# Kernel optimization log

Measured on AMD Instinct MI355X. Metric: run time of the kernel, lower is better.

## Reference

```python
import jax, jax.numpy as jnp
import numpy as np

B, T, S = 64, 48, 48
E, H, L, V = 512, 1024, 2, 32000


def setup_inputs() -> dict:
    key = jax.random.key(0)
    ks = jax.random.split(key, 16)
    s = 0.02
    return {
        "tgt_input": jax.random.randint(ks[0], (B, T), 0, V),
        "h0": jax.random.normal(ks[1], (L, B, H), jnp.float32),
        "c0": jax.random.normal(ks[2], (L, B, H), jnp.float32),
        "encoder_output": jax.random.normal(ks[3], (B, S, H), jnp.float32),
        "src_key_padding_mask": jnp.zeros((B, S), bool),
        "embedding": jax.random.normal(ks[4], (V, E), jnp.float32) * s,
        "W_l": jax.random.normal(ks[5], (H, H), jnp.float32) * s,
        "b_l": jnp.zeros((H,), jnp.float32),
        "W_ih0": jax.random.normal(ks[6], (4 * H, E + H), jnp.float32) * s,
        "W_hh0": jax.random.normal(ks[7], (4 * H, H), jnp.float32) * s,
        "b_ih0": jnp.zeros((4 * H,), jnp.float32),
        "b_hh0": jnp.zeros((4 * H,), jnp.float32),
        "W_ih1": jax.random.normal(ks[8], (4 * H, H), jnp.float32) * s,
        "W_hh1": jax.random.normal(ks[9], (4 * H, H), jnp.float32) * s,
        "b_ih1": jnp.zeros((4 * H,), jnp.float32),
        "b_hh1": jnp.zeros((4 * H,), jnp.float32),
    }


def _lstm_cell(x, h, c, W_ih, W_hh, b_ih, b_hh):
    # PyTorch gate order: i, f, g, o
    gates = x @ W_ih.T + b_ih + h @ W_hh.T + b_hh  # [B, 4H]
    i, f, g, o = jnp.split(gates, 4, axis=-1)
    c_new = jax.nn.sigmoid(f) * c + jax.nn.sigmoid(i) * jnp.tanh(g)
    h_new = jax.nn.sigmoid(o) * jnp.tanh(c_new)
    return h_new, c_new


def reference(tgt_input, h0, c0, encoder_output, src_key_padding_mask,
              embedding, W_l, b_l,
              W_ih0, W_hh0, b_ih0, b_hh0,
              W_ih1, W_hh1, b_ih1, b_hh1):
    emb = embedding[tgt_input]              # [B, T, E]
    emb_t = jnp.transpose(emb, (1, 0, 2))   # [T, B, E]
    layers = ((W_ih0, W_hh0, b_ih0, b_hh0), (W_ih1, W_hh1, b_ih1, b_hh1))

    def step(carry, x_t):
        h, c = carry                        # [L, B, H] each
        # Luong attention with query = last-layer hidden state
        q = h[-1] @ W_l.T + b_l             # [B, H]
        scores = jnp.einsum('bh,bsh->bs', q, encoder_output)
        scores = jnp.where(src_key_padding_mask, -jnp.inf, scores)
        attn = jax.nn.softmax(scores, axis=-1)
        ctx = jnp.einsum('bs,bsh->bh', attn, encoder_output)  # [B, H]
        x = jnp.concatenate([x_t, ctx], axis=-1)              # [B, E+H]
        new_h, new_c = [], []
        for l, (W_ih, W_hh, b_ih, b_hh) in enumerate(layers):
            hn, cn = _lstm_cell(x, h[l], c[l], W_ih, W_hh, b_ih, b_hh)
            new_h.append(hn)
            new_c.append(cn)
            x = hn
        return (jnp.stack(new_h), jnp.stack(new_c)), x  # x = top-layer output

    (hn, cn), outs = jax.lax.scan(step, (h0, c0), emb_t)
    outputs = jnp.transpose(outs, (1, 0, 2))  # [B, T, H]
    return outputs, hn, cn
```

## Files before the change

kernel.cpp:

```cpp
#include <hip/hip_runtime.h>
#include <stdint.h>


using short8 = __attribute__((ext_vector_type(8))) short;
using f32x4  = __attribute__((ext_vector_type(4))) float;
typedef unsigned short u16;
typedef unsigned long long u64;

#define B_  64
#define T_  48
#define S_  48
#define H_  1024
#define E_  512

__device__ __forceinline__ float bf2f(u16 u) {
    union { unsigned int i; float f; } v; v.i = ((unsigned int)u) << 16; return v.f;
}
__device__ __forceinline__ u16 f2bf(float f) {
    union { float f; unsigned int i; } v; v.f = f;
    unsigned int r = v.i + 0x7fff + ((v.i >> 16) & 1);
    return (u16)(r >> 16);
}
__device__ __forceinline__ float sigm(float x) { return 1.f / (1.f + __expf(-x)); }


__global__ void cast_copy(u16* __restrict__ dst, int dld, int doff,
                          const float* __restrict__ src, int sld, int soff,
                          int rows, int colshift) {
    int cols = 1 << colshift;
    int total = rows << colshift;
    for (int i = blockIdx.x * blockDim.x + threadIdx.x; i < total;
         i += gridDim.x * blockDim.x) {
        int r = i >> colshift, c = i & (cols - 1);
        dst[(size_t)r * dld + doff + c] = f2bf(src[(size_t)r * sld + soff + c]);
    }
}

__global__ void transpose_cast(u16* __restrict__ dst, const float* __restrict__ src) {
    int idx = blockIdx.x * blockDim.x + threadIdx.x;
    int r = idx >> 10, c = idx & 1023;
    dst[idx] = f2bf(src[(size_t)c * 1024 + r]);
}

__global__ void embed_gather(u16* __restrict__ embA, const float* __restrict__ emb,
                             const int* __restrict__ tgt) {
    int row = blockIdx.x;
    int t = row >> 6, b = row & 63;
    int id = tgt[b * T_ + t];
    const float* s = emb + (size_t)id * E_;
    u16* d = embA + (size_t)row * E_;
    for (int e = threadIdx.x; e < E_; e += blockDim.x) d[e] = f2bf(s[e]);
}

__global__ void sbias_kernel(float* __restrict__ sbias, const float* __restrict__ enc,
                             const float* __restrict__ b_l) {
    int r = blockIdx.x, lane = threadIdx.x;
    const float* e = enc + (size_t)r * H_;
    float acc = 0.f;
    for (int k = lane; k < H_; k += 64) acc += b_l[k] * e[k];
    for (int o = 32; o; o >>= 1) acc += __shfl_xor(acc, o);
    if (lane == 0) sbias[r] = acc;
}

__global__ void init_state(u16* __restrict__ xa0_0, u16* __restrict__ xa1_0,
                           const float* __restrict__ h0) {
    int i = blockIdx.x * blockDim.x + threadIdx.x;
    int l = i >> 16, rem = i & 65535, b = rem >> 10, c = rem & 1023;
    u16 hb = f2bf(h0[i]);
    if (l == 0) xa0_0[b * 2048 + 1024 + c] = hb;
    else        xa1_0[b * 2048 + 1024 + c] = hb;
}

__global__ __launch_bounds__(256) void gemm64(
    const u16* __restrict__ A, const u16* __restrict__ W, u16* __restrict__ D,
    const float* __restrict__ bias1, const float* __restrict__ bias2,
    int N, int Kd)
{
    __shared__ float part[4][64][65];
    int tid = threadIdx.x, w = tid >> 6, lane = tid & 63;
    int hf = lane >> 4, q = lane & 15;
    int n0 = blockIdx.x * 64, m0 = blockIdx.y * 64;
    int ks = Kd >> 2;
    int kb = w * ks + hf * 8;
    const u16* ap = A + (size_t)(m0 + q) * Kd + kb;
    const u16* wp = W + (size_t)(n0 + q) * Kd + kb;
    f32x4 acc[4][4] = {};
    for (int k0 = 0; k0 < ks; k0 += 32) {
        short8 bf[4], af[4];
#pragma unroll
        for (int n = 0; n < 4; ++n) bf[n] = *(const short8*)(wp + (size_t)n * 16 * Kd + k0);
#pragma unroll
        for (int m = 0; m < 4; ++m) af[m] = *(const short8*)(ap + (size_t)m * 16 * Kd + k0);
#pragma unroll
        for (int m = 0; m < 4; ++m)
#pragma unroll
            for (int n = 0; n < 4; ++n)
                acc[m][n] = __builtin_amdgcn_mfma_f32_16x16x32_bf16(af[m], bf[n], acc[m][n], 0, 0, 0);
    }
#pragma unroll
    for (int m = 0; m < 4; ++m)
#pragma unroll
        for (int n = 0; n < 4; ++n)
#pragma unroll
            for (int r = 0; r < 4; ++r)
                part[w][m * 16 + hf * 4 + r][n * 16 + q] = acc[m][n][r];
    __syncthreads();
#pragma unroll
    for (int k = 0; k < 16; ++k) {
        int o = tid + k * 256;
        int row = o >> 6, col = o & 63;
        float v = part[0][row][col] + part[1][row][col]
                + part[2][row][col] + part[3][row][col];
        if (bias1) v += bias1[n0 + col] + bias2[n0 + col];
        D[(size_t)(m0 + row) * N + n0 + col] = f2bf(v);
    }
}


struct PParams {
    const float *W_ih0, *W_hh0, *W_ih1, *W_hh1;
    const u16  *preG, *encW, *encB;
    const float *sbias, *b_ih1, *b_hh1, *c0in;
    const unsigned char* mask;
    u16 *XA0, *XA1;
    float *out, *hn0, *hn1, *cn0, *cn1;
    unsigned *cnt, *flags;
};

__device__ __forceinline__ void gridarrive(unsigned* cnt, int ep, int g) {
    __syncthreads();
    if (threadIdx.x == 0)
        __hip_atomic_fetch_add(&cnt[g * 256 + ep], 1u,
                               __ATOMIC_RELAXED, __HIP_MEMORY_SCOPE_AGENT);
    asm volatile("" ::: "memory");
}
__device__ __forceinline__ void gridpoll(unsigned* cnt, unsigned* flags,
                                         int ep, int g) {
    if (blockIdx.x == 0) {
        if (threadIdx.x < 64) {
            int spin = 0;
            for (;;) {
                unsigned v = __hip_atomic_load(&cnt[threadIdx.x * 256 + ep],
                                               __ATOMIC_RELAXED,
                                               __HIP_MEMORY_SCOPE_AGENT);
                if (__ballot(v >= 4u) == ~0ull) break;
                if (++spin > (1 << 20)) break;
            }
            __hip_atomic_store(&flags[threadIdx.x * 256 + ep], 1u,
                               __ATOMIC_RELAXED, __HIP_MEMORY_SCOPE_AGENT);
        }
    } else if (threadIdx.x == 0) {
        int spin = 0;
        while (!__hip_atomic_load(&flags[g * 256 + ep], __ATOMIC_RELAXED,
                                  __HIP_MEMORY_SCOPE_AGENT)) {
            if (++spin > (1 << 20)) break;
        }
    }
    asm volatile("" ::: "memory");
    __syncthreads();
}

__global__ void __launch_bounds__(256, 1) decoder_persistent(PParams P) {
    __shared__ u16 wlds[2][4096][8];
    __shared__ union {
        struct { float h1f[1056]; float sc[48][4]; float pr[48]; } at;
        float gates[64][20];
    } sm;

    const int tid = threadIdx.x, blk = blockIdx.x;
    const int w = tid >> 6, lane = tid & 63, g4 = lane >> 4, q = lane & 15;
    const int b2 = tid >> 2, j2 = tid & 3;
    const int colg = blk * 4 + j2;

    {
        int r = tid & 15, cb = tid >> 4;
        int grow = (r >> 2) * 1024 + blk * 4 + (r & 3);
#pragma unroll
        for (int l = 0; l < 2; ++l) {
            const float* Sa = l ? P.W_ih1 : P.W_ih0;
            const float* Sb = l ? P.W_hh1 : P.W_hh0;
            int sld  = l ? 1024 : 1536;
            int soff = l ? 0 : 512;
            for (int it = 0; it < 16; ++it) {
                int c = cb + it * 16;
                int k = c * 8;
                const float* src = (k < 1024)
                    ? (Sa + (size_t)grow * sld + soff + k)
                    : (Sb + (size_t)grow * 1024 + (k - 1024));
                float4 x0 = *(const float4*)(src);
                float4 x1 = *(const float4*)(src + 4);
                short8 v;
                v[0] = f2bf(x0.x); v[1] = f2bf(x0.y); v[2] = f2bf(x0.z); v[3] = f2bf(x0.w);
                v[4] = f2bf(x1.x); v[5] = f2bf(x1.y); v[6] = f2bf(x1.z); v[7] = f2bf(x1.w);
                *(short8*)&wlds[l][c * 16 + r][0] = v;
            }
        }
    }
    __syncthreads();
    float bsum[4];
#pragma unroll
    for (int g = 0; g < 4; ++g)
        bsum[g] = P.b_ih1[g * 1024 + colg] + P.b_hh1[g * 1024 + colg];
    float c0r = P.c0in[b2 * 1024 + colg];
    float c1r = P.c0in[65536 + b2 * 1024 + colg];

    const int ab = (blk & 7) * 8 + ((blk >> 3) & 7);
    const int aq = blk >> 6;
    int ep = 0;
    int t = 0;

    auto gemm_half = [&](const u16* Abase, int layer, int kbase, f32x4 seed) -> f32x4 {
        const u16* ap = Abase + (size_t)(w * 16 + q) * 2048 + kbase + g4 * 8;
        short8 xa[32];
#pragma unroll
        for (int kk = 0; kk < 32; ++kk)
            xa[kk] = *(const short8*)(ap + kk * 32);
        f32x4 a0 = seed, a1 = {}, a2 = {}, a3 = {};
        const int cbs = (kbase >> 3) + g4;
#pragma unroll
        for (int kk = 0; kk < 32; kk += 4) {
            a0 = __builtin_amdgcn_mfma_f32_16x16x32_bf16(
                xa[kk + 0], *(const short8*)&wlds[layer][(cbs + (kk + 0) * 4) * 16 + q][0], a0, 0, 0, 0);
            a1 = __builtin_amdgcn_mfma_f32_16x16x32_bf16(
                xa[kk + 1], *(const short8*)&wlds[layer][(cbs + (kk + 1) * 4) * 16 + q][0], a1, 0, 0, 0);
            a2 = __builtin_amdgcn_mfma_f32_16x16x32_bf16(
                xa[kk + 2], *(const short8*)&wlds[layer][(cbs + (kk + 2) * 4) * 16 + q][0], a2, 0, 0, 0);
            a3 = __builtin_amdgcn_mfma_f32_16x16x32_bf16(
                xa[kk + 3], *(const short8*)&wlds[layer][(cbs + (kk + 3) * 4) * 16 + q][0], a3, 0, 0, 0);
        }
        return (a0 + a1) + (a2 + a3);
    };

    auto lstm_phase = [&](const u16* Abase, int layer, f32x4 seed,
                          float add0, float add1, float add2, float add3,
                          float& creg, u16* dA, u16* dB, float* outp,
                          float* hnO, float* cnO, int doLast) {
        f32x4 g = gemm_half(Abase, layer, 0, seed);
#pragma unroll
        for (int r = 0; r < 4; ++r) sm.gates[w * 16 + g4 * 4 + r][q] = g[r];
        __syncthreads();
        float gi = sm.gates[b2][j2]      + add0;
        float gf = sm.gates[b2][4 + j2]  + add1;
        float gg = sm.gates[b2][8 + j2]  + add2;
        float go = sm.gates[b2][12 + j2] + add3;
        float cnew = sigm(gf) * creg + sigm(gi) * tanhf(gg);
        float hnew = sigm(go) * tanhf(cnew);
        creg = cnew;
        ((u16*)&sm.gates[b2][16])[j2] = f2bf(hnew);
        if (outp) outp[(size_t)(b2 * T_ + t) * H_ + colg] = hnew;
        if (doLast) { hnO[b2 * 1024 + colg] = hnew; cnO[b2 * 1024 + colg] = cnew; }
        __syncthreads();
        if (tid < 64) {
            u64 pk;
            __builtin_memcpy(&pk, (const u16*)&sm.gates[tid][16], 8);
            __hip_atomic_store((u64*)(dA + tid * 2048 + blk * 4), pk,
                               __ATOMIC_RELAXED, __HIP_MEMORY_SCOPE_AGENT);
            if (dB)
                __hip_atomic_store((u64*)(dB + tid * 2048 + blk * 4), pk,
                                   __ATOMIC_RELAXED, __HIP_MEMORY_SCOPE_AGENT);
        }
    };

    f32x4 g0p = gemm_half(P.XA0, 0, 1024, f32x4{});
    f32x4 g1p = {};

    for (t = 0; t < T_; ++t) {
        const int last = (t == T_ - 1);
        u16* xa0c = P.XA0 + (size_t)t * 131072;
        u16* xa0n = P.XA0 + (size_t)(t + 1) * 131072;
        u16* xa1c = P.XA1 + (size_t)t * 131072;
        u16* xa1n = P.XA1 + (size_t)(t + 1) * 131072;

        for (int i = tid; i < H_; i += 256)
            sm.at.h1f[(i >> 8) * 264 + (i & 255)] = bf2f(xa1c[ab * 2048 + 1024 + i]);
        __syncthreads();
        if (tid < 192) {
            int s = tid >> 2, kq = tid & 3;
            const u16* ew = P.encW + ((size_t)ab * S_ + s) * H_ + kq * 256;
            const float2* hp = (const float2*)(sm.at.h1f + kq * 264);
            float p0 = 0.f, p1 = 0.f, p2 = 0.f, p3 = 0.f;
#pragma unroll
            for (int k = 0; k < 256; k += 32) {
                short8 v0 = *(const short8*)(ew + k);
                short8 v1 = *(const short8*)(ew + k + 8);
                short8 v2 = *(const short8*)(ew + k + 16);
                short8 v3 = *(const short8*)(ew + k + 24);
#pragma unroll
                for (int e = 0; e < 8; e += 2) {
                    float2 h0v = hp[(k >> 1) + (e >> 1)];
                    p0 += h0v.x * bf2f(((u16*)&v0)[e]) + h0v.y * bf2f(((u16*)&v0)[e + 1]);
                    float2 h1v = hp[(k >> 1) + 4 + (e >> 1)];
                    p1 += h1v.x * bf2f(((u16*)&v1)[e]) + h1v.y * bf2f(((u16*)&v1)[e + 1]);
                    float2 h2v = hp[(k >> 1) + 8 + (e >> 1)];
                    p2 += h2v.x * bf2f(((u16*)&v2)[e]) + h2v.y * bf2f(((u16*)&v2)[e + 1]);
                    float2 h3v = hp[(k >> 1) + 12 + (e >> 1)];
                    p3 += h3v.x * bf2f(((u16*)&v3)[e]) + h3v.y * bf2f(((u16*)&v3)[e + 1]);
                }
            }
            sm.at.sc[s][kq] = (p0 + p1) + (p2 + p3);
        }
        __syncthreads();
        if (tid < 64) {
            float v = -3.0e38f;
            if (tid < S_) {
                v = sm.at.sc[tid][0] + sm.at.sc[tid][1] + sm.at.sc[tid][2]
                  + sm.at.sc[tid][3] + P.sbias[ab * S_ + tid];
                if (P.mask[ab * S_ + tid]) v = -3.0e38f;
            }
            float mx = v;
            for (int o = 32; o; o >>= 1) mx = fmaxf(mx, __shfl_xor(mx, o));
            float e = (tid < S_) ? __expf(v - mx) : 0.f;
            float su = e;
            for (int o = 32; o; o >>= 1) su += __shfl_xor(su, o);
            if (tid < S_) sm.at.pr[tid] = e / su;
        }
        __syncthreads();
        {
            int col = aq * 256 + tid;
            const u16* eb = P.encB + (size_t)ab * S_ * H_ + col;
            float a0 = 0.f, a1 = 0.f, a2 = 0.f, a3 = 0.f;
#pragma unroll
            for (int s = 0; s < 48; s += 4) {
                a0 += sm.at.pr[s + 0] * bf2f(eb[(size_t)(s + 0) * H_]);
                a1 += sm.at.pr[s + 1] * bf2f(eb[(size_t)(s + 1) * H_]);
                a2 += sm.at.pr[s + 2] * bf2f(eb[(size_t)(s + 2) * H_]);
                a3 += sm.at.pr[s + 3] * bf2f(eb[(size_t)(s + 3) * H_]);
            }
            u16 myb = f2bf((a0 + a1) + (a2 + a3));
            int other = __shfl_xor((int)myb, 1);
            if ((tid & 1) == 0) {
                unsigned pk = (unsigned)myb | ((unsigned)(u16)other << 16);
                __hip_atomic_store((unsigned*)(xa0c + ab * 2048 + col), pk,
                                   __ATOMIC_RELAXED, __HIP_MEMORY_SCOPE_AGENT);
            }
        }
        gridarrive(P.cnt, ++ep, ab);
        const u16* pgp = P.preG + ((size_t)t * 64 + b2) * 4096 + colg;
        u16 pg0 = pgp[0], pg1 = pgp[1024], pg2 = pgp[2048], pg3 = pgp[3072];
        gridpoll(P.cnt, P.flags, ep, ab);

        lstm_phase(xa0c, 0, g0p, bf2f(pg0), bf2f(pg1), bf2f(pg2), bf2f(pg3),
                   c0r, xa1c, xa0n + 1024, nullptr, P.hn0, P.cn0, last);
        gridarrive(P.cnt, ++ep, ab);
        g1p = gemm_half(xa1c, 1, 1024, f32x4{});
        gridpoll(P.cnt, P.flags, ep, ab);

        lstm_phase(xa1c, 1, g1p, bsum[0], bsum[1], bsum[2], bsum[3],
                   c1r, xa1n + 1024, nullptr, P.out, P.hn1, P.cn1, last);
        gridarrive(P.cnt, ++ep, ab);
        g0p = gemm_half(xa0n, 0, 1024, f32x4{});
        gridpoll(P.cnt, P.flags, ep, ab);
    }
}


extern "C" void kernel_launch(void* const* d_in, const int* in_sizes, int n_in,
                              void* d_out, int out_size, void* d_ws, size_t ws_size,
                              hipStream_t stream) {
    const int*   tgt      = (const int*)d_in[0];
    const float* h0       = (const float*)d_in[1];
    const float* c0in     = (const float*)d_in[2];
    const float* enc      = (const float*)d_in[3];
    const unsigned char* mask = (const unsigned char*)d_in[4];
    const float* embedding= (const float*)d_in[5];
    const float* W_l      = (const float*)d_in[6];
    const float* b_l      = (const float*)d_in[7];
    const float* W_ih0    = (const float*)d_in[8];
    const float* W_hh0    = (const float*)d_in[9];
    const float* b_ih0    = (const float*)d_in[10];
    const float* b_hh0    = (const float*)d_in[11];
    const float* W_ih1    = (const float*)d_in[12];
    const float* W_hh1    = (const float*)d_in[13];
    const float* b_ih1    = (const float*)d_in[14];
    const float* b_hh1    = (const float*)d_in[15];
    float* out = (float*)d_out;

    char* ws = (char*)d_ws;
    u16* W0emb = (u16*)ws;               ws += (size_t)4096 * 512 * 2;
    u16* WlT   = (u16*)ws;               ws += (size_t)1024 * 1024 * 2;
    u16* embA  = (u16*)ws;               ws += (size_t)3072 * 512 * 2;
    u16* encB  = (u16*)ws;               ws += (size_t)3072 * 1024 * 2;
    u16* encWb = (u16*)ws;               ws += (size_t)3072 * 1024 * 2;
    float* sbias = (float*)ws;           ws += (size_t)3072 * 4;
    u16* preG  = (u16*)ws;               ws += (size_t)3072 * 4096 * 2;
    u16* XA0   = (u16*)ws;               ws += (size_t)49 * 131072 * 2;
    u16* XA1   = (u16*)ws;               ws += (size_t)49 * 131072 * 2;
    unsigned* bar = (unsigned*)ws;       ws += 262144;

    cast_copy<<<2048, 256, 0, stream>>>(W0emb, 512, 0, W_ih0, 1536, 0, 4096, 9);
    cast_copy<<<2048, 256, 0, stream>>>(encB, 1024, 0, enc, 1024, 0, 3072, 10);
    transpose_cast<<<4096, 256, 0, stream>>>(WlT, W_l);
    embed_gather<<<3072, 256, 0, stream>>>(embA, embedding, tgt);
    init_state<<<512, 256, 0, stream>>>(XA0, XA1, h0);
    sbias_kernel<<<3072, 64, 0, stream>>>(sbias, enc, b_l);
    gemm64<<<dim3(64, 48), 256, 0, stream>>>(embA, W0emb, preG, b_ih0, b_hh0, 4096, 512);
    gemm64<<<dim3(16, 48), 256, 0, stream>>>(encB, WlT, encWb, nullptr, nullptr, 1024, 1024);
    hipMemsetAsync(bar, 0, 262144, stream);

    PParams prm;
    prm.W_ih0 = W_ih0; prm.W_hh0 = W_hh0; prm.W_ih1 = W_ih1; prm.W_hh1 = W_hh1;
    prm.preG = preG; prm.encW = encWb; prm.encB = encB;
    prm.sbias = sbias; prm.b_ih1 = b_ih1; prm.b_hh1 = b_hh1; prm.c0in = c0in;
    prm.mask = mask;
    prm.XA0 = XA0; prm.XA1 = XA1;
    prm.out = out;
    prm.hn0 = out + 3145728; prm.hn1 = out + 3145728 + 65536;
    prm.cn0 = out + 3276800; prm.cn1 = out + 3276800 + 65536;
    prm.cnt = bar; prm.flags = bar + 16384;
    decoder_persistent<<<256, 256, 0, stream>>>(prm);

    (void)in_sizes; (void)n_in; (void)out_size; (void)ws_size;
}
```

Baseline: 1.322 ms.

## Replace master-block barrier with hierarchical atomic counter and overlap layer-1 GEMM

The grid barrier drops the scheme where block 0 polls 64 group counters and writes per-group flags. Instead, the last arriving block of each 4-block group increments a global counter that every block polls directly, removing one relay hop per barrier. The layer-1 hidden-state GEMM (gemm_half on xa1c) is moved earlier so it runs while waiting at the attention barrier, and the barrier that used to follow it is left with nothing to hide. This adds contention on a single polled counter and relies on xa1c already being complete at that point.

Result: slower. 1.482 ms (+12.1%).

```diff
diff --git a/kernel.cpp b/kernel.cpp
--- a/kernel.cpp
+++ b/kernel.cpp
@@ -124,35 +124,27 @@
     const unsigned char* mask;
     u16 *XA0, *XA1;
     float *out, *hn0, *hn1, *cn0, *cn1;
-    unsigned *cnt, *flags;
+    unsigned *cnt, *gcnt;
 };
 
-__device__ __forceinline__ void gridarrive(unsigned* cnt, int ep, int g) {
+__device__ __forceinline__ void gridarrive(unsigned* cnt, unsigned* gcnt,
+                                           int ep, int g) {
     __syncthreads();
-    if (threadIdx.x == 0)
-        __hip_atomic_fetch_add(&cnt[g * 256 + ep], 1u,
-                               __ATOMIC_RELAXED, __HIP_MEMORY_SCOPE_AGENT);
+    if (threadIdx.x == 0) {
+        unsigned old = __hip_atomic_fetch_add(&cnt[g * 256 + ep], 1u,
+                                              __ATOMIC_RELAXED,
+                                              __HIP_MEMORY_SCOPE_AGENT);
+        if (old == 3u)
+            __hip_atomic_fetch_add(&gcnt[ep * 16], 1u,
+                                   __ATOMIC_RELAXED, __HIP_MEMORY_SCOPE_AGENT);
+    }
     asm volatile("" ::: "memory");
 }
-__device__ __forceinline__ void gridpoll(unsigned* cnt, unsigned* flags,
-                                         int ep, int g) {
-    if (blockIdx.x == 0) {
-        if (threadIdx.x < 64) {
-            int spin = 0;
-            for (;;) {
-                unsigned v = __hip_atomic_load(&cnt[threadIdx.x * 256 + ep],
-                                               __ATOMIC_RELAXED,
-                                               __HIP_MEMORY_SCOPE_AGENT);
-                if (__ballot(v >= 4u) == ~0ull) break;
-                if (++spin > (1 << 20)) break;
-            }
-            __hip_atomic_store(&flags[threadIdx.x * 256 + ep], 1u,
-                               __ATOMIC_RELAXED, __HIP_MEMORY_SCOPE_AGENT);
-        }
-    } else if (threadIdx.x == 0) {
+__device__ __forceinline__ void gridpoll(unsigned* gcnt, int ep) {
+    if (threadIdx.x == 0) {
         int spin = 0;
-        while (!__hip_atomic_load(&flags[g * 256 + ep], __ATOMIC_RELAXED,
-                                  __HIP_MEMORY_SCOPE_AGENT)) {
+        while (__hip_atomic_load(&gcnt[ep * 16], __ATOMIC_RELAXED,
+                                 __HIP_MEMORY_SCOPE_AGENT) < 64u) {
             if (++spin > (1 << 20)) break;
         }
     }
@@ -334,22 +326,22 @@
                                    __ATOMIC_RELAXED, __HIP_MEMORY_SCOPE_AGENT);
             }
         }
-        gridarrive(P.cnt, ++ep, ab);
+        gridarrive(P.cnt, P.gcnt, ++ep, ab);
         const u16* pgp = P.preG + ((size_t)t * 64 + b2) * 4096 + colg;
         u16 pg0 = pgp[0], pg1 = pgp[1024], pg2 = pgp[2048], pg3 = pgp[3072];
-        gridpoll(P.cnt, P.flags, ep, ab);
+        g1p = gemm_half(xa1c, 1, 1024, f32x4{});
+        gridpoll(P.gcnt, ep);
 
         lstm_phase(xa0c, 0, g0p, bf2f(pg0), bf2f(pg1), bf2f(pg2), bf2f(pg3),
                    c0r, xa1c, xa0n + 1024, nullptr, P.hn0, P.cn0, last);
-        gridarrive(P.cnt, ++ep, ab);
-        g1p = gemm_half(xa1c, 1, 1024, f32x4{});
-        gridpoll(P.cnt, P.flags, ep, ab);
+        gridarrive(P.cnt, P.gcnt, ++ep, ab);
+        gridpoll(P.gcnt, ep);
 
         lstm_phase(xa1c, 1, g1p, bsum[0], bsum[1], bsum[2], bsum[3],
                    c1r, xa1n + 1024, nullptr, P.out, P.hn1, P.cn1, last);
-        gridarrive(P.cnt, ++ep, ab);
+        gridarrive(P.cnt, P.gcnt, ++ep, ab);
         g0p = gemm_half(xa0n, 0, 1024, f32x4{});
-        gridpoll(P.cnt, P.flags, ep, ab);
+        gridpoll(P.gcnt, ep);
     }
 }
 
@@ -406,7 +398,7 @@
     prm.out = out;
     prm.hn0 = out + 3145728; prm.hn1 = out + 3145728 + 65536;
     prm.cn0 = out + 3276800; prm.cn1 = out + 3276800 + 65536;
-    prm.cnt = bar; prm.flags = bar + 16384;
+    prm.cnt = bar; prm.gcnt = bar + 16384;
     decoder_persistent<<<256, 256, 0, stream>>>(prm);
 
     (void)in_sizes; (void)n_in; (void)out_size; (void)ws_size;
```
